# Kernel optimization log

Measured on AMD Instinct MI355X. Metric: run time of the kernel, lower is better.

## Reference

```python
import jax, jax.numpy as jnp
import numpy as np

EPS = 1e-5

def _batchnorm(h, gamma, beta):
    # training-mode BatchNorm1d over node dim, biased variance
    mu = jnp.mean(h, axis=0)
    var = jnp.mean((h - mu) ** 2, axis=0)
    return (h - mu) * jax.lax.rsqrt(var + EPS) * gamma + beta

def _sage(x, src, dst, n, Wl, b, Wr):
    # sum-aggregate source features into destinations, then linear + root linear
    agg = jax.ops.segment_sum(x[src], dst, num_segments=n)  # [N, F]
    return agg @ Wl + b + x @ Wr

def setup_inputs() -> dict:
    key = jax.random.key(0)
    ks = jax.random.split(key, 8)
    N, E, F, H, O = 200000, 1200000, 64, 128, 128
    s = lambda fan_in: 1.0 / np.sqrt(fan_in)
    return {
        "x": jax.random.normal(ks[0], (N, F), jnp.float32),
        "edge_index": jax.random.randint(ks[1], (2, E), 0, N, jnp.int64),
        "W1l": jax.random.normal(ks[2], (F, H), jnp.float32) * s(F),
        "b1": jnp.zeros((H,), jnp.float32),
        "W1r": jax.random.normal(ks[3], (F, H), jnp.float32) * s(F),
        "g1": jnp.ones((H,), jnp.float32),
        "be1": jnp.zeros((H,), jnp.float32),
        "W2l": jax.random.normal(ks[4], (H, O), jnp.float32) * s(H),
        "b2": jnp.zeros((O,), jnp.float32),
        "W2r": jax.random.normal(ks[5], (H, O), jnp.float32) * s(H),
        "g2": jnp.ones((O,), jnp.float32),
        "be2": jnp.zeros((O,), jnp.float32),
    }

def reference(x, edge_index, W1l, b1, W1r, g1, be1, W2l, b2, W2r, g2, be2):
    n = x.shape[0]
    src, dst = edge_index[0], edge_index[1]
    h = jax.nn.relu(_sage(x, src, dst, n, W1l, b1, W1r))
    h = _batchnorm(h, g1, be1)
    h = jax.nn.relu(_sage(h, src, dst, n, W2l, b2, W2r))
    h = _batchnorm(h, g2, be2)
    return jax.nn.relu(h)
```

## Files before the change

### kernel.cpp

```cpp
#include <hip/hip_runtime.h>

#define N_NODES 200000
#define N_EDGES 1200000
#define F_IN    64
#define F_H     128
#define BN_EPS  1e-5f

typedef short bf16x8 __attribute__((ext_vector_type(8)));
typedef float f32x4  __attribute__((ext_vector_type(4)));
typedef unsigned short us4 __attribute__((ext_vector_type(4)));

__device__ __forceinline__ unsigned short f2bf(float f) {
    union { float f; unsigned u; } v; v.f = f;
    unsigned r = (v.u + 0x7FFFu + ((v.u >> 16) & 1u)) >> 16;
    return (unsigned short)r;
}
__device__ __forceinline__ float bf2f(unsigned short b) {
    union { unsigned u; float f; } v; v.u = ((unsigned)b) << 16;
    return v.f;
}

__global__ void pack_weights_kernel(const float* __restrict__ W,
                                    const float* __restrict__ kscale,
                                    short* __restrict__ P, int KT)
{
    int t = blockIdx.x * 256 + threadIdx.x;
    if (t >= 8 * KT * 64) return;
    int lane = t & 63;
    int kt   = (t >> 6) % KT;
    int nt   = t / (64 * KT);
    int k0   = kt * 32 + (lane >> 4) * 8;
    int n    = nt * 16 + (lane & 15);
#pragma unroll
    for (int j = 0; j < 8; ++j) {
        float w = W[(size_t)(k0 + j) * 128 + n];
        if (kscale) w *= kscale[k0 + j];
        P[(size_t)t * 8 + j] = (short)f2bf(w);
    }
}

__global__ __launch_bounds__(256) void hist_kernel(const int* __restrict__ ei,
                                                   int* __restrict__ deg, int E)
{
    int e = blockIdx.x * 256 + threadIdx.x;
    if (e < E) atomicAdd(&deg[ei[E + e]], 1);
}

__global__ __launch_bounds__(256) void scan1_kernel(const int* __restrict__ deg,
        int* __restrict__ part, int* __restrict__ bsum, int n)
{
    __shared__ int s[256];
    int t = threadIdx.x;
    int base = blockIdx.x * 1024 + t * 4;
    int v[4];
#pragma unroll
    for (int j = 0; j < 4; ++j) v[j] = (base + j < n) ? deg[base + j] : 0;
    int tsum = v[0] + v[1] + v[2] + v[3];
    s[t] = tsum;
    __syncthreads();
    for (int off = 1; off < 256; off <<= 1) {
        int xv = (t >= off) ? s[t - off] : 0;
        __syncthreads();
        s[t] += xv;
        __syncthreads();
    }
    int excl = s[t] - tsum;
#pragma unroll
    for (int j = 0; j < 4; ++j) {
        if (base + j < n) part[base + j] = excl;
        excl += v[j];
    }
    if (t == 255) bsum[blockIdx.x] = s[255];
}

__global__ void scan2_kernel(int* __restrict__ bsum, int nb)
{
    __shared__ int s[256];
    int t = threadIdx.x;
    int v = (t < nb) ? bsum[t] : 0;
    s[t] = v;
    __syncthreads();
    for (int off = 1; off < 256; off <<= 1) {
        int xv = (t >= off) ? s[t - off] : 0;
        __syncthreads();
        s[t] += xv;
        __syncthreads();
    }
    if (t < nb) bsum[t] = s[t] - v;
}

__global__ __launch_bounds__(256) void scan3_kernel(
    const int* __restrict__ part, const int* __restrict__ bsum,
    const int* __restrict__ deg, int* __restrict__ rowptr,
    int* __restrict__ cursor, float* __restrict__ degf, int n, int E)
{
    int i = blockIdx.x * 256 + threadIdx.x;
    if (i == 0) rowptr[n] = E;
    if (i >= n) return;
    int r = part[i] + bsum[i >> 10];
    rowptr[i] = r;
    cursor[i] = r;
    degf[i]   = (float)deg[i];
}

__global__ __launch_bounds__(256) void fill_kernel(const int* __restrict__ ei,
        int* __restrict__ cursor, int* __restrict__ ssrc, int E)
{
    int e = blockIdx.x * 256 + threadIdx.x;
    if (e >= E) return;
    int d = ei[E + e];
    int pos = atomicAdd(&cursor[d], 1);
    ssrc[pos] = ei[e];
}

__global__ __launch_bounds__(256) void gather1_kernel(
    const float* __restrict__ x, const int* __restrict__ rowptr,
    const int* __restrict__ ssrc, unsigned short* __restrict__ aggb)
{
    const int tid  = threadIdx.x;
    const int wv   = tid >> 6;
    const int lane = tid & 63;
    const int sub  = lane >> 4;
    const int li   = lane & 15;
    const int row  = blockIdx.x * 16 + wv * 4 + sub;

    int b = rowptr[row], e = rowptr[row + 1];
    float4 acc = {0.f, 0.f, 0.f, 0.f};
    if (b < e) {
        int s = ssrc[b];
        for (int j = b; j < e; ++j) {
            int sn = (j + 1 < e) ? ssrc[j + 1] : 0;
            float4 v = ((const float4*)(x + (size_t)s * F_IN))[li];
            acc.x += v.x; acc.y += v.y; acc.z += v.z; acc.w += v.w;
            s = sn;
        }
    }
    us4 o;
    o.x = f2bf(acc.x); o.y = f2bf(acc.y); o.z = f2bf(acc.z); o.w = f2bf(acc.w);
    *(us4*)(aggb + (size_t)row * F_IN + li * 4) = o;
}

__global__ __launch_bounds__(256) void gather2_kernel(
    const unsigned short* __restrict__ t1, const int* __restrict__ rowptr,
    const int* __restrict__ ssrc, unsigned short* __restrict__ aggb)
{
    const int tid  = threadIdx.x;
    const int wv   = tid >> 6;
    const int lane = tid & 63;
    const int sub  = lane >> 4;
    const int li   = lane & 15;
    const int row  = blockIdx.x * 16 + wv * 4 + sub;

    int b = rowptr[row], e = rowptr[row + 1];
    float acc[8] = {};
    if (b < e) {
        int s = ssrc[b];
        for (int j = b; j < e; ++j) {
            int sn = (j + 1 < e) ? ssrc[j + 1] : 0;
            bf16x8 v = *(const bf16x8*)(t1 + (size_t)s * F_H + li * 8);
#pragma unroll
            for (int k = 0; k < 8; ++k) acc[k] += bf2f((unsigned short)v[k]);
            s = sn;
        }
    }
    bf16x8 o;
#pragma unroll
    for (int k = 0; k < 8; ++k) o[k] = (short)f2bf(acc[k]);
    *(bf16x8*)(aggb + (size_t)row * F_H + li * 8) = o;
}

template<int K, bool L2>
__global__ __launch_bounds__(256) void gemm_mfma_kernel(
    const unsigned short* __restrict__ Ab,
    const float* __restrict__ Xf,
    const unsigned short* __restrict__ Xb,
    const bf16x8* __restrict__ Wlp, const bf16x8* __restrict__ Wrp,
    const float* __restrict__ bias,
    const float* __restrict__ c2, const float* __restrict__ degf,
    float* __restrict__ outF, unsigned short* __restrict__ outB,
    float* __restrict__ gsum, float* __restrict__ gsq)
{
    constexpr int KT = K / 32;
    __shared__ float sS[128];
    __shared__ float sQ[128];

    const int tid  = threadIdx.x;
    const int lane = tid & 63;
    const int wv   = tid >> 6;
    const int m    = lane & 15;
    const int quad = lane >> 4;
    const int rowbase = blockIdx.x * 256 + wv * 64;

    if (tid < 128) { sS[tid] = 0.f; sQ[tid] = 0.f; }

    float bcol[8], ccol[8];
#pragma unroll
    for (int nt = 0; nt < 8; ++nt) {
        bcol[nt] = bias[nt * 16 + m];
        if constexpr (L2) ccol[nt] = c2[nt * 16 + m];
    }

    f32x4 acc[4][8] = {};

#pragma unroll
    for (int kt = 0; kt < KT; ++kt) {
        const int k0 = kt * 32 + quad * 8;
        bf16x8 af[4], xf[4];
#pragma unroll
        for (int st = 0; st < 4; ++st) {
            int r  = rowbase + st * 16 + m;
            int rc = r < N_NODES ? r : N_NODES - 1;
            af[st] = *(const bf16x8*)(Ab + (size_t)rc * K + k0);
            if constexpr (L2) {
                xf[st] = *(const bf16x8*)(Xb + (size_t)rc * K + k0);
            } else {
                const float4* xp = (const float4*)(Xf + (size_t)rc * K + k0);
                float4 x0 = xp[0], x1 = xp[1];
                xf[st][0] = (short)f2bf(x0.x); xf[st][1] = (short)f2bf(x0.y);
                xf[st][2] = (short)f2bf(x0.z); xf[st][3] = (short)f2bf(x0.w);
                xf[st][4] = (short)f2bf(x1.x); xf[st][5] = (short)f2bf(x1.y);
                xf[st][6] = (short)f2bf(x1.z); xf[st][7] = (short)f2bf(x1.w);
            }
        }
#pragma unroll
        for (int nt = 0; nt < 8; ++nt) {
            bf16x8 wl = Wlp[(nt * KT + kt) * 64 + lane];
#pragma unroll
            for (int st = 0; st < 4; ++st)
                acc[st][nt] = __builtin_amdgcn_mfma_f32_16x16x32_bf16(
                    af[st], wl, acc[st][nt], 0, 0, 0);
            bf16x8 wr = Wrp[(nt * KT + kt) * 64 + lane];
#pragma unroll
            for (int st = 0; st < 4; ++st)
                acc[st][nt] = __builtin_amdgcn_mfma_f32_16x16x32_bf16(
                    xf[st], wr, acc[st][nt], 0, 0, 0);
        }
    }

    __syncthreads();

    float stS[8] = {}, stQ[8] = {};
#pragma unroll
    for (int st = 0; st < 4; ++st) {
        const int orow = rowbase + st * 16 + quad * 4;
        float dg[4];
        if constexpr (L2) {
#pragma unroll
            for (int r = 0; r < 4; ++r) {
                int rr = orow + r;
                dg[r] = (rr < N_NODES) ? degf[rr] : 0.f;
            }
        }
#pragma unroll
        for (int nt = 0; nt < 8; ++nt) {
            int col = nt * 16 + m;
#pragma unroll
            for (int r = 0; r < 4; ++r) {
                int rr = orow + r;
                if (rr < N_NODES) {
                    float base = L2 ? fmaf(dg[r], ccol[nt], bcol[nt]) : bcol[nt];
                    float v = fmaxf(acc[st][nt][r] + base, 0.f);
                    if constexpr (L2) outF[(size_t)rr * 128 + col] = v;
                    else              outB[(size_t)rr * 128 + col] = f2bf(v);
                    stS[nt] += v;
                    stQ[nt] = fmaf(v, v, stQ[nt]);
                }
            }
        }
    }

#pragma unroll
    for (int nt = 0; nt < 8; ++nt) {
        atomicAdd(&sS[nt * 16 + m], stS[nt]);
        atomicAdd(&sQ[nt * 16 + m], stQ[nt]);
    }
    __syncthreads();
    const int rep = (blockIdx.x & 3) * 128;
    if (tid < 128) {
        atomicAdd(&gsum[rep + tid], sS[tid]);
        atomicAdd(&gsq[rep + tid],  sQ[tid]);
    }
}

__global__ void bn_finalize_kernel(
    const float* __restrict__ gsum, const float* __restrict__ gsq,
    const float* __restrict__ g, const float* __restrict__ be,
    float* __restrict__ scale, float* __restrict__ shift, float invN)
{
    int c = threadIdx.x;
    float s = gsum[c] + gsum[128 + c] + gsum[256 + c] + gsum[384 + c];
    float q = gsq[c]  + gsq[128 + c]  + gsq[256 + c]  + gsq[384 + c];
    float mean = s * invN;
    float var  = fmaxf(q * invN - mean * mean, 0.f);
    float sc   = g[c] * rsqrtf(var + BN_EPS);
    scale[c] = sc;
    shift[c] = be[c] - mean * sc;
}

__global__ void bn_fold_kernel(
    const float* __restrict__ shift1, const float* __restrict__ W2l,
    const float* __restrict__ W2r, const float* __restrict__ b2,
    float* __restrict__ c2, float* __restrict__ crb)
{
    int col = threadIdx.x;
    float a = 0.f, r = 0.f;
    for (int k = 0; k < 128; ++k) {
        float s = shift1[k];
        a = fmaf(s, W2l[(size_t)k * 128 + col], a);
        r = fmaf(s, W2r[(size_t)k * 128 + col], r);
    }
    c2[col]  = a;
    crb[col] = r + b2[col];
}

__global__ __launch_bounds__(256) void bn_apply_relu_kernel(
    float* __restrict__ h, const float* __restrict__ scale,
    const float* __restrict__ shift, int n4)
{
    int i = blockIdx.x * 256 + threadIdx.x;
    if (i >= n4) return;
    int cb = i & 31;
    float4 v  = ((float4*)h)[i];
    float4 sc = ((const float4*)scale)[cb];
    float4 sh = ((const float4*)shift)[cb];
    v.x = fmaxf(fmaf(v.x, sc.x, sh.x), 0.f);
    v.y = fmaxf(fmaf(v.y, sc.y, sh.y), 0.f);
    v.z = fmaxf(fmaf(v.z, sc.z, sh.z), 0.f);
    v.w = fmaxf(fmaf(v.w, sc.w, sh.w), 0.f);
    ((float4*)h)[i] = v;
}

extern "C" void kernel_launch(void* const* d_in, const int* in_sizes, int n_in,
                              void* d_out, int out_size, void* d_ws, size_t ws_size,
                              hipStream_t stream) {
    const float* x   = (const float*)d_in[0];
    const int*   ei  = (const int*)d_in[1];
    const float* W1l = (const float*)d_in[2];
    const float* b1  = (const float*)d_in[3];
    const float* W1r = (const float*)d_in[4];
    const float* g1  = (const float*)d_in[5];
    const float* be1 = (const float*)d_in[6];
    const float* W2l = (const float*)d_in[7];
    const float* b2  = (const float*)d_in[8];
    const float* W2r = (const float*)d_in[9];
    const float* g2  = (const float*)d_in[10];
    const float* be2 = (const float*)d_in[11];
    float* out = (float*)d_out;

    const int N = N_NODES, E = N_EDGES;
    const int NB1 = (N + 1023) / 1024;
    const int nT  = (N + 255) / 256;

    float* ws     = (float*)d_ws;
    float* gsum1  = ws;          float* gsq1   = ws + 512;
    float* gsum2  = ws + 1024;   float* gsq2   = ws + 1536;
    float* scale1 = ws + 2048;   float* shift1 = ws + 2176;
    float* scale2 = ws + 2304;   float* shift2 = ws + 2432;
    float* c2v    = ws + 2560;   float* crb    = ws + 2688;
    short* W1lp = (short*)(ws + 3072);
    short* W1rp = (short*)(ws + 3072 + 4096);
    short* W2lp = (short*)(ws + 3072 + 8192);
    short* W2rp = (short*)(ws + 3072 + 16384);
    int*   deg    = (int*)(ws + 27648);
    int*   part   = deg + N;
    int*   bsum   = part + N;
    int*   rowptr = bsum + 1024;
    int*   cursor = rowptr + (N + 1024);
    float* degf   = (float*)(cursor + N);
    int*   ssrc   = (int*)(degf + N);
    unsigned short* t1   = (unsigned short*)(ssrc + E);
    unsigned short* aggb = t1 + (size_t)N * F_H;

    hipMemsetAsync(ws, 0, 2048 * sizeof(float), stream);
    hipMemsetAsync(deg, 0, (size_t)N * sizeof(int), stream);
    pack_weights_kernel<<<4, 256, 0, stream>>>(W1l, nullptr, W1lp, 2);
    pack_weights_kernel<<<4, 256, 0, stream>>>(W1r, nullptr, W1rp, 2);
    hist_kernel<<<(E + 255) / 256, 256, 0, stream>>>(ei, deg, E);
    scan1_kernel<<<NB1, 256, 0, stream>>>(deg, part, bsum, N);
    scan2_kernel<<<1, 256, 0, stream>>>(bsum, NB1);
    scan3_kernel<<<(N + 255) / 256, 256, 0, stream>>>(part, bsum, deg, rowptr,
                                                      cursor, degf, N, E);
    fill_kernel<<<(E + 255) / 256, 256, 0, stream>>>(ei, cursor, ssrc, E);

    gather1_kernel<<<N / 16, 256, 0, stream>>>(x, rowptr, ssrc, aggb);
    gemm_mfma_kernel<F_IN, false><<<nT, 256, 0, stream>>>(
        aggb, x, nullptr, (const bf16x8*)W1lp, (const bf16x8*)W1rp, b1,
        nullptr, nullptr, nullptr, t1, gsum1, gsq1);
    bn_finalize_kernel<<<1, 128, 0, stream>>>(gsum1, gsq1, g1, be1,
                                              scale1, shift1, 1.f / N);

    pack_weights_kernel<<<8, 256, 0, stream>>>(W2l, scale1, W2lp, 4);
    pack_weights_kernel<<<8, 256, 0, stream>>>(W2r, scale1, W2rp, 4);
    bn_fold_kernel<<<1, 128, 0, stream>>>(shift1, W2l, W2r, b2, c2v, crb);
    gather2_kernel<<<N / 16, 256, 0, stream>>>(t1, rowptr, ssrc, aggb);
    gemm_mfma_kernel<F_H, true><<<nT, 256, 0, stream>>>(
        aggb, nullptr, t1, (const bf16x8*)W2lp, (const bf16x8*)W2rp, crb,
        c2v, degf, out, nullptr, gsum2, gsq2);
    bn_finalize_kernel<<<1, 128, 0, stream>>>(gsum2, gsq2, g2, be2,
                                              scale2, shift2, 1.f / N);
    bn_apply_relu_kernel<<<(N * F_H / 4 + 255) / 256, 256, 0, stream>>>(
        out, scale2, shift2, N * F_H / 4);
}
```

Baseline: 660.1 us.

## Unroll gather loops by four and shrink GEMM tile with register prefetch

Both gather kernels now issue four independent neighbor-row loads per iteration, using masked FMA weights and prefetching the next four source indices, so more memory requests are in flight per row. The fused GEMM kernel's row tile drops from 256 to 128 rows per block with a launch-bounds occupancy hint of 2. Its K loop double-buffers the A/X fragment loads in registers so the next step's loads overlap the current MFMAs. The costs are more padded loads for low-degree rows, twice as many GEMM blocks and more atomics on the batch-norm statistics.

```diff
diff --git a/kernel.cpp b/kernel.cpp
--- a/kernel.cpp
+++ b/kernel.cpp
@@ -124,16 +124,37 @@
     const int li   = lane & 15;
     const int row  = blockIdx.x * 16 + wv * 4 + sub;
 
-    int b = rowptr[row], e = rowptr[row + 1];
+    const int b = rowptr[row], e = rowptr[row + 1];
     float4 acc = {0.f, 0.f, 0.f, 0.f};
-    if (b < e) {
-        int s = ssrc[b];
-        for (int j = b; j < e; ++j) {
-            int sn = (j + 1 < e) ? ssrc[j + 1] : 0;
-            float4 v = ((const float4*)(x + (size_t)s * F_IN))[li];
-            acc.x += v.x; acc.y += v.y; acc.z += v.z; acc.w += v.w;
-            s = sn;
-        }
+    int s0 = row, s1 = row, s2 = row, s3 = row;
+    if (b + 0 < e) s0 = ssrc[b + 0];
+    if (b + 1 < e) s1 = ssrc[b + 1];
+    if (b + 2 < e) s2 = ssrc[b + 2];
+    if (b + 3 < e) s3 = ssrc[b + 3];
+    for (int j = b; j < e; j += 4) {
+        int n0 = row, n1 = row, n2 = row, n3 = row;
+        int jn = j + 4;
+        if (jn + 0 < e) n0 = ssrc[jn + 0];
+        if (jn + 1 < e) n1 = ssrc[jn + 1];
+        if (jn + 2 < e) n2 = ssrc[jn + 2];
+        if (jn + 3 < e) n3 = ssrc[jn + 3];
+        float4 v0 = ((const float4*)(x + (size_t)s0 * F_IN))[li];
+        float4 v1 = ((const float4*)(x + (size_t)s1 * F_IN))[li];
+        float4 v2 = ((const float4*)(x + (size_t)s2 * F_IN))[li];
+        float4 v3 = ((const float4*)(x + (size_t)s3 * F_IN))[li];
+        float w0 = (j + 0 < e) ? 1.f : 0.f;
+        float w1 = (j + 1 < e) ? 1.f : 0.f;
+        float w2 = (j + 2 < e) ? 1.f : 0.f;
+        float w3 = (j + 3 < e) ? 1.f : 0.f;
+        acc.x = fmaf(v0.x, w0, acc.x); acc.y = fmaf(v0.y, w0, acc.y);
+        acc.z = fmaf(v0.z, w0, acc.z); acc.w = fmaf(v0.w, w0, acc.w);
+        acc.x = fmaf(v1.x, w1, acc.x); acc.y = fmaf(v1.y, w1, acc.y);
+        acc.z = fmaf(v1.z, w1, acc.z); acc.w = fmaf(v1.w, w1, acc.w);
+        acc.x = fmaf(v2.x, w2, acc.x); acc.y = fmaf(v2.y, w2, acc.y);
+        acc.z = fmaf(v2.z, w2, acc.z); acc.w = fmaf(v2.w, w2, acc.w);
+        acc.x = fmaf(v3.x, w3, acc.x); acc.y = fmaf(v3.y, w3, acc.y);
+        acc.z = fmaf(v3.z, w3, acc.z); acc.w = fmaf(v3.w, w3, acc.w);
+        s0 = n0; s1 = n1; s2 = n2; s3 = n3;
     }
     us4 o;
     o.x = f2bf(acc.x); o.y = f2bf(acc.y); o.z = f2bf(acc.z); o.w = f2bf(acc.w);
@@ -151,17 +172,36 @@
     const int li   = lane & 15;
     const int row  = blockIdx.x * 16 + wv * 4 + sub;
 
-    int b = rowptr[row], e = rowptr[row + 1];
+    const int b = rowptr[row], e = rowptr[row + 1];
     float acc[8] = {};
-    if (b < e) {
-        int s = ssrc[b];
-        for (int j = b; j < e; ++j) {
-            int sn = (j + 1 < e) ? ssrc[j + 1] : 0;
-            bf16x8 v = *(const bf16x8*)(t1 + (size_t)s * F_H + li * 8);
-#pragma unroll
-            for (int k = 0; k < 8; ++k) acc[k] += bf2f((unsigned short)v[k]);
-            s = sn;
+    int s0 = row, s1 = row, s2 = row, s3 = row;
+    if (b + 0 < e) s0 = ssrc[b + 0];
+    if (b + 1 < e) s1 = ssrc[b + 1];
+    if (b + 2 < e) s2 = ssrc[b + 2];
+    if (b + 3 < e) s3 = ssrc[b + 3];
+    for (int j = b; j < e; j += 4) {
+        int n0 = row, n1 = row, n2 = row, n3 = row;
+        int jn = j + 4;
+        if (jn + 0 < e) n0 = ssrc[jn + 0];
+        if (jn + 1 < e) n1 = ssrc[jn + 1];
+        if (jn + 2 < e) n2 = ssrc[jn + 2];
+        if (jn + 3 < e) n3 = ssrc[jn + 3];
+        bf16x8 v0 = *(const bf16x8*)(t1 + (size_t)s0 * F_H + li * 8);
+        bf16x8 v1 = *(const bf16x8*)(t1 + (size_t)s1 * F_H + li * 8);
+        bf16x8 v2 = *(const bf16x8*)(t1 + (size_t)s2 * F_H + li * 8);
+        bf16x8 v3 = *(const bf16x8*)(t1 + (size_t)s3 * F_H + li * 8);
+        float w0 = (j + 0 < e) ? 1.f : 0.f;
+        float w1 = (j + 1 < e) ? 1.f : 0.f;
+        float w2 = (j + 2 < e) ? 1.f : 0.f;
+        float w3 = (j + 3 < e) ? 1.f : 0.f;
+#pragma unroll
+        for (int k = 0; k < 8; ++k) {
+            acc[k] = fmaf(bf2f((unsigned short)v0[k]), w0, acc[k]);
+            acc[k] = fmaf(bf2f((unsigned short)v1[k]), w1, acc[k]);
+            acc[k] = fmaf(bf2f((unsigned short)v2[k]), w2, acc[k]);
+            acc[k] = fmaf(bf2f((unsigned short)v3[k]), w3, acc[k]);
         }
+        s0 = n0; s1 = n1; s2 = n2; s3 = n3;
     }
     bf16x8 o;
 #pragma unroll
@@ -170,7 +210,7 @@
 }
 
 template<int K, bool L2>
-__global__ __launch_bounds__(256) void gemm_mfma_kernel(
+__global__ __launch_bounds__(256, 2) void gemm_mfma_kernel(
     const unsigned short* __restrict__ Ab,
     const float* __restrict__ Xf,
     const unsigned short* __restrict__ Xb,
@@ -189,9 +229,16 @@
     const int wv   = tid >> 6;
     const int m    = lane & 15;
     const int quad = lane >> 4;
-    const int rowbase = blockIdx.x * 256 + wv * 64;
+    const int rowbase = blockIdx.x * 128 + wv * 32;
 
     if (tid < 128) { sS[tid] = 0.f; sQ[tid] = 0.f; }
+
+    int rc[2];
+#pragma unroll
+    for (int st = 0; st < 2; ++st) {
+        int r = rowbase + st * 16 + m;
+        rc[st] = r < N_NODES ? r : N_NODES - 1;
+    }
 
     float bcol[8], ccol[8];
 #pragma unroll
@@ -200,21 +247,17 @@
         if constexpr (L2) ccol[nt] = c2[nt * 16 + m];
     }
 
-    f32x4 acc[4][8] = {};
-
-#pragma unroll
-    for (int kt = 0; kt < KT; ++kt) {
+    f32x4 acc[2][8] = {};
+
+    auto load_kt = [&](int kt, bf16x8 af[2], bf16x8 xf[2]) {
         const int k0 = kt * 32 + quad * 8;
-        bf16x8 af[4], xf[4];
-#pragma unroll
-        for (int st = 0; st < 4; ++st) {
-            int r  = rowbase + st * 16 + m;
-            int rc = r < N_NODES ? r : N_NODES - 1;
-            af[st] = *(const bf16x8*)(Ab + (size_t)rc * K + k0);
+#pragma unroll
+        for (int st = 0; st < 2; ++st) {
+            af[st] = *(const bf16x8*)(Ab + (size_t)rc[st] * K + k0);
             if constexpr (L2) {
-                xf[st] = *(const bf16x8*)(Xb + (size_t)rc * K + k0);
+                xf[st] = *(const bf16x8*)(Xb + (size_t)rc[st] * K + k0);
             } else {
-                const float4* xp = (const float4*)(Xf + (size_t)rc * K + k0);
+                const float4* xp = (const float4*)(Xf + (size_t)rc[st] * K + k0);
                 float4 x0 = xp[0], x1 = xp[1];
                 xf[st][0] = (short)f2bf(x0.x); xf[st][1] = (short)f2bf(x0.y);
                 xf[st][2] = (short)f2bf(x0.z); xf[st][3] = (short)f2bf(x0.w);
@@ -222,26 +265,36 @@
                 xf[st][6] = (short)f2bf(x1.z); xf[st][7] = (short)f2bf(x1.w);
             }
         }
+    };
+
+    bf16x8 aCur[2], xCur[2];
+    load_kt(0, aCur, xCur);
+#pragma unroll
+    for (int kt = 0; kt < KT; ++kt) {
+        bf16x8 aNxt[2], xNxt[2];
+        if (kt + 1 < KT) load_kt(kt + 1, aNxt, xNxt);
 #pragma unroll
         for (int nt = 0; nt < 8; ++nt) {
             bf16x8 wl = Wlp[(nt * KT + kt) * 64 + lane];
 #pragma unroll
-            for (int st = 0; st < 4; ++st)
+            for (int st = 0; st < 2; ++st)
                 acc[st][nt] = __builtin_amdgcn_mfma_f32_16x16x32_bf16(
-                    af[st], wl, acc[st][nt], 0, 0, 0);
+                    aCur[st], wl, acc[st][nt], 0, 0, 0);
             bf16x8 wr = Wrp[(nt * KT + kt) * 64 + lane];
 #pragma unroll
-            for (int st = 0; st < 4; ++st)
+            for (int st = 0; st < 2; ++st)
                 acc[st][nt] = __builtin_amdgcn_mfma_f32_16x16x32_bf16(
-                    xf[st], wr, acc[st][nt], 0, 0, 0);
+                    xCur[st], wr, acc[st][nt], 0, 0, 0);
         }
+#pragma unroll
+        for (int st = 0; st < 2; ++st) { aCur[st] = aNxt[st]; xCur[st] = xNxt[st]; }
     }
 
     __syncthreads();
 
     float stS[8] = {}, stQ[8] = {};
 #pragma unroll
-    for (int st = 0; st < 4; ++st) {
+    for (int st = 0; st < 2; ++st) {
         const int orow = rowbase + st * 16 + quad * 4;
         float dg[4];
         if constexpr (L2) {
@@ -349,7 +402,7 @@
 
     const int N = N_NODES, E = N_EDGES;
     const int NB1 = (N + 1023) / 1024;
-    const int nT  = (N + 255) / 256;
+    const int nT  = (N + 127) / 128;
 
     float* ws     = (float*)d_ws;
     float* gsum1  = ws;          float* gsq1   = ws + 512;
```

Result: faster. 622.1 us (-5.8%).

## Batch gather index loads and prefetch GEMM rows into registers with smaller tiles

Applied to the files above, without the earlier changes.

The gather kernels now load eight neighbor indices and eight feature rows per iteration and use masked FMAs, which puts more memory requests in flight and replaces the serial one-edge-at-a-time chain. The GEMM kernel halves rows per block (128 instead of 256), preloads all A and X fragments for every k-step into registers before the MFMA loop, and asks for two blocks per SIMD through launch bounds to raise occupancy. The cost is extra wasted loads for padded edges, which fetch the node's own row with weight zero, higher register pressure, and twice as many GEMM blocks, each doing its own BN-stat atomics.

```diff
diff --git a/kernel.cpp b/kernel.cpp
--- a/kernel.cpp
+++ b/kernel.cpp
@@ -124,16 +124,30 @@
     const int li   = lane & 15;
     const int row  = blockIdx.x * 16 + wv * 4 + sub;
 
-    int b = rowptr[row], e = rowptr[row + 1];
+    const int b = rowptr[row], e = rowptr[row + 1];
     float4 acc = {0.f, 0.f, 0.f, 0.f};
-    if (b < e) {
-        int s = ssrc[b];
-        for (int j = b; j < e; ++j) {
-            int sn = (j + 1 < e) ? ssrc[j + 1] : 0;
-            float4 v = ((const float4*)(x + (size_t)s * F_IN))[li];
-            acc.x += v.x; acc.y += v.y; acc.z += v.z; acc.w += v.w;
-            s = sn;
-        }
+    int s[8];
+#pragma unroll
+    for (int q = 0; q < 8; ++q) s[q] = (b + q < e) ? ssrc[b + q] : row;
+    for (int j = b; j < e; j += 8) {
+        int nn[8];
+        const int jn = j + 8;
+#pragma unroll
+        for (int q = 0; q < 8; ++q) nn[q] = (jn + q < e) ? ssrc[jn + q] : row;
+        float4 v[8];
+#pragma unroll
+        for (int q = 0; q < 8; ++q)
+            v[q] = ((const float4*)(x + (size_t)s[q] * F_IN))[li];
+#pragma unroll
+        for (int q = 0; q < 8; ++q) {
+            float w = (j + q < e) ? 1.f : 0.f;
+            acc.x = fmaf(v[q].x, w, acc.x);
+            acc.y = fmaf(v[q].y, w, acc.y);
+            acc.z = fmaf(v[q].z, w, acc.z);
+            acc.w = fmaf(v[q].w, w, acc.w);
+        }
+#pragma unroll
+        for (int q = 0; q < 8; ++q) s[q] = nn[q];
     }
     us4 o;
     o.x = f2bf(acc.x); o.y = f2bf(acc.y); o.z = f2bf(acc.z); o.w = f2bf(acc.w);
@@ -151,17 +165,29 @@
     const int li   = lane & 15;
     const int row  = blockIdx.x * 16 + wv * 4 + sub;
 
-    int b = rowptr[row], e = rowptr[row + 1];
+    const int b = rowptr[row], e = rowptr[row + 1];
     float acc[8] = {};
-    if (b < e) {
-        int s = ssrc[b];
-        for (int j = b; j < e; ++j) {
-            int sn = (j + 1 < e) ? ssrc[j + 1] : 0;
-            bf16x8 v = *(const bf16x8*)(t1 + (size_t)s * F_H + li * 8);
-#pragma unroll
-            for (int k = 0; k < 8; ++k) acc[k] += bf2f((unsigned short)v[k]);
-            s = sn;
-        }
+    int s[8];
+#pragma unroll
+    for (int q = 0; q < 8; ++q) s[q] = (b + q < e) ? ssrc[b + q] : row;
+    for (int j = b; j < e; j += 8) {
+        int nn[8];
+        const int jn = j + 8;
+#pragma unroll
+        for (int q = 0; q < 8; ++q) nn[q] = (jn + q < e) ? ssrc[jn + q] : row;
+        bf16x8 v[8];
+#pragma unroll
+        for (int q = 0; q < 8; ++q)
+            v[q] = *(const bf16x8*)(t1 + (size_t)s[q] * F_H + li * 8);
+#pragma unroll
+        for (int q = 0; q < 8; ++q) {
+            float w = (j + q < e) ? 1.f : 0.f;
+#pragma unroll
+            for (int k = 0; k < 8; ++k)
+                acc[k] = fmaf(bf2f((unsigned short)v[q][k]), w, acc[k]);
+        }
+#pragma unroll
+        for (int q = 0; q < 8; ++q) s[q] = nn[q];
     }
     bf16x8 o;
 #pragma unroll
@@ -170,7 +196,7 @@
 }
 
 template<int K, bool L2>
-__global__ __launch_bounds__(256) void gemm_mfma_kernel(
+__global__ __launch_bounds__(256, 2) void gemm_mfma_kernel(
     const unsigned short* __restrict__ Ab,
     const float* __restrict__ Xf,
     const unsigned short* __restrict__ Xb,
@@ -189,9 +215,58 @@
     const int wv   = tid >> 6;
     const int m    = lane & 15;
     const int quad = lane >> 4;
-    const int rowbase = blockIdx.x * 256 + wv * 64;
+    const int rowbase = blockIdx.x * 128 + wv * 32;
 
     if (tid < 128) { sS[tid] = 0.f; sQ[tid] = 0.f; }
+
+    int rc[2];
+#pragma unroll
+    for (int st = 0; st < 2; ++st) {
+        int r = rowbase + st * 16 + m;
+        rc[st] = r < N_NODES ? r : N_NODES - 1;
+    }
+
+    bf16x8 aReg[2][KT], xReg[2][KT];
+#pragma unroll
+    for (int st = 0; st < 2; ++st) {
+        const unsigned short* ap = Ab + (size_t)rc[st] * K + quad * 8;
+#pragma unroll
+        for (int kt = 0; kt < KT; ++kt)
+            aReg[st][kt] = *(const bf16x8*)(ap + kt * 32);
+    }
+    if constexpr (L2) {
+#pragma unroll
+        for (int st = 0; st < 2; ++st) {
+            const unsigned short* xp = Xb + (size_t)rc[st] * K + quad * 8;
+#pragma unroll
+            for (int kt = 0; kt < KT; ++kt)
+                xReg[st][kt] = *(const bf16x8*)(xp + kt * 32);
+        }
+    } else {
+        float4 xr[2][KT][2];
+#pragma unroll
+        for (int st = 0; st < 2; ++st) {
+            const float* xp = Xf + (size_t)rc[st] * K + quad * 8;
+#pragma unroll
+            for (int kt = 0; kt < KT; ++kt) {
+                xr[st][kt][0] = *(const float4*)(xp + kt * 32);
+                xr[st][kt][1] = *(const float4*)(xp + kt * 32 + 4);
+            }
+        }
+#pragma unroll
+        for (int st = 0; st < 2; ++st)
+#pragma unroll
+            for (int kt = 0; kt < KT; ++kt) {
+                xReg[st][kt][0] = (short)f2bf(xr[st][kt][0].x);
+                xReg[st][kt][1] = (short)f2bf(xr[st][kt][0].y);
+                xReg[st][kt][2] = (short)f2bf(xr[st][kt][0].z);
+                xReg[st][kt][3] = (short)f2bf(xr[st][kt][0].w);
+                xReg[st][kt][4] = (short)f2bf(xr[st][kt][1].x);
+                xReg[st][kt][5] = (short)f2bf(xr[st][kt][1].y);
+                xReg[st][kt][6] = (short)f2bf(xr[st][kt][1].z);
+                xReg[st][kt][7] = (short)f2bf(xr[st][kt][1].w);
+            }
+    }
 
     float bcol[8], ccol[8];
 #pragma unroll
@@ -200,40 +275,22 @@
         if constexpr (L2) ccol[nt] = c2[nt * 16 + m];
     }
 
-    f32x4 acc[4][8] = {};
+    f32x4 acc[2][8] = {};
 
 #pragma unroll
     for (int kt = 0; kt < KT; ++kt) {
-        const int k0 = kt * 32 + quad * 8;
-        bf16x8 af[4], xf[4];
-#pragma unroll
-        for (int st = 0; st < 4; ++st) {
-            int r  = rowbase + st * 16 + m;
-            int rc = r < N_NODES ? r : N_NODES - 1;
-            af[st] = *(const bf16x8*)(Ab + (size_t)rc * K + k0);
-            if constexpr (L2) {
-                xf[st] = *(const bf16x8*)(Xb + (size_t)rc * K + k0);
-            } else {
-                const float4* xp = (const float4*)(Xf + (size_t)rc * K + k0);
-                float4 x0 = xp[0], x1 = xp[1];
-                xf[st][0] = (short)f2bf(x0.x); xf[st][1] = (short)f2bf(x0.y);
-                xf[st][2] = (short)f2bf(x0.z); xf[st][3] = (short)f2bf(x0.w);
-                xf[st][4] = (short)f2bf(x1.x); xf[st][5] = (short)f2bf(x1.y);
-                xf[st][6] = (short)f2bf(x1.z); xf[st][7] = (short)f2bf(x1.w);
-            }
-        }
 #pragma unroll
         for (int nt = 0; nt < 8; ++nt) {
             bf16x8 wl = Wlp[(nt * KT + kt) * 64 + lane];
 #pragma unroll
-            for (int st = 0; st < 4; ++st)
+            for (int st = 0; st < 2; ++st)
                 acc[st][nt] = __builtin_amdgcn_mfma_f32_16x16x32_bf16(
-                    af[st], wl, acc[st][nt], 0, 0, 0);
+                    aReg[st][kt], wl, acc[st][nt], 0, 0, 0);
             bf16x8 wr = Wrp[(nt * KT + kt) * 64 + lane];
 #pragma unroll
-            for (int st = 0; st < 4; ++st)
+            for (int st = 0; st < 2; ++st)
                 acc[st][nt] = __builtin_amdgcn_mfma_f32_16x16x32_bf16(
-                    xf[st], wr, acc[st][nt], 0, 0, 0);
+                    xReg[st][kt], wr, acc[st][nt], 0, 0, 0);
         }
     }
 
@@ -241,7 +298,7 @@
 
     float stS[8] = {}, stQ[8] = {};
 #pragma unroll
-    for (int st = 0; st < 4; ++st) {
+    for (int st = 0; st < 2; ++st) {
         const int orow = rowbase + st * 16 + quad * 4;
         float dg[4];
         if constexpr (L2) {
@@ -349,7 +406,7 @@
 
     const int N = N_NODES, E = N_EDGES;
     const int NB1 = (N + 1023) / 1024;
-    const int nT  = (N + 255) / 256;
+    const int nT  = (N + 127) / 128;
 
     float* ws     = (float*)d_ws;
     float* gsum1  = ws;          float* gsq1   = ws + 512;
```

Result: faster. 607.1 us (-8.0%).
